# Optimization experiments

Measured on AMD Instinct MI355X. Metric: run time of the kernel, lower is better.

The kernel has to match this reference:

```python
import jax, jax.numpy as jnp
import numpy as np
from jax import lax

EPS = 1e-7  # keras.backend.epsilon()
DT = 0.05

def _k(a):
    # (3,3) -> HWIO (3,3,1,1) fp32 kernel constant
    return jnp.asarray(np.asarray(a, dtype=np.float32).reshape(3, 3, 1, 1))

KXP = _k([[0,0,0],[0,-1,1],[0,0,0]])
KXN = _k([[0,0,0],[-1,1,0],[0,0,0]])
KYP = _k([[0,1,0],[0,-1,0],[0,0,0]])
KYN = _k([[0,0,0],[0,1,0],[0,-1,0]])
KXC = _k([[0,0,0],[-1,0,1],[0,0,0]])
KYC = _k([[0,1,0],[0,0,0],[0,-1,0]])
KLX = _k([[1,0,-1],[2,0,-2],[1,0,-1]])
KLY = _k([[1,2,1],[0,0,0],[-1,-2,-1]])

def conv(x, k):
    # TF K.conv2d 'same' == XLA cross-correlation, NHWC/HWIO
    return lax.conv_general_dilated(x, k, (1, 1), 'SAME',
                                    dimension_numbers=('NHWC', 'HWIO', 'NHWC'))

def setup_inputs() -> dict:
    key = jax.random.key(0)
    k1, k2 = jax.random.split(key)
    B, H, W = 32, 512, 512
    u = jax.random.normal(k1, (B, H, W, 1), dtype=jnp.float32)
    img = jax.random.uniform(k2, (B, H, W, 1), dtype=jnp.float32)
    alpha = jnp.ones((1, 1, 1, 1), jnp.float32)
    beta = jnp.ones((1, 1, 1, 1), jnp.float32)
    gamma = jnp.ones((1, 1, 1, 1), jnp.float32)
    return {"u": u, "img": img, "alpha": alpha, "beta": beta, "gamma": gamma}

def reference(u, img, alpha, beta, gamma):
    # --- edge stopping function g(img) (precomputed in build() in original) ---
    ex = conv(img, KLX)
    ey = conv(img, KLY)
    edges = jnp.square(jnp.square(ex) + jnp.square(ey))
    edges = edges / jnp.max(edges)
    edges = 1.0 / (edges + 1.0)
    gex = conv(edges, KXC)
    gey = conv(edges, KYC)
    # --- upwind transport term ---
    xp = conv(u, KXP); xn = conv(u, KXN)
    yp = conv(u, KYP); yn = conv(u, KYN)
    fxp = jax.nn.relu(gex); fxn = -jax.nn.relu(-gex)
    fyp = jax.nn.relu(gey); fyn = -jax.nn.relu(-gey)
    transport = 20.0 * ((fxp * xp + fxn * xn) + (fyp * yp + fyn * yn))
    # --- curvature (divergence of normalized gradient) ---
    gux = conv(u, KXC)
    guy = conv(u, KYC)
    normu = jnp.sqrt(jnp.square(gux) + jnp.square(guy) + EPS)
    kappa = conv(gux / (normu + EPS), KXC) + conv(guy / (normu + EPS), KYC)
    curvature = edges * kappa * normu
    balloon = edges * normu
    return u + DT * (curvature * alpha + transport * beta + balloon * gamma)
```

## Files before the change

### kernel.cpp

```cpp
#include <hip/hip_runtime.h>

#define HH 512
#define WW 512
#define EPSF 1e-7f
#define DTF 0.05f
#define RS1 4
#define RSF 8
#define PANW 256

__device__ __forceinline__ float bperm(int addr, float v) {
    return __int_as_float(__builtin_amdgcn_ds_bpermute(addr, __float_as_int(v)));
}

struct R10 { float v[10]; };
struct Raw10 { float4 a, b; };

__device__ __forceinline__ void issue_row10(const float* __restrict__ base, int row,
                                            int lane, Raw10& r) {
    if ((unsigned)row < (unsigned)HH) {
        const float4* p = (const float4*)(base + (size_t)row * WW + 8 * lane);
        r.a = p[0]; r.b = p[1];
    } else {
        r.a = make_float4(0.f, 0.f, 0.f, 0.f);
        r.b = make_float4(0.f, 0.f, 0.f, 0.f);
    }
}

__device__ __forceinline__ void finish_row10(const Raw10& q, int bpu, int bpd,
                                             bool lo, bool hi, R10& r) {
    r.v[1] = q.a.x; r.v[2] = q.a.y; r.v[3] = q.a.z; r.v[4] = q.a.w;
    r.v[5] = q.b.x; r.v[6] = q.b.y; r.v[7] = q.b.z; r.v[8] = q.b.w;
    float l = bperm(bpu, r.v[8]);
    float h = bperm(bpd, r.v[1]);
    r.v[0] = lo ? 0.f : l;
    r.v[9] = hi ? 0.f : h;
}

__global__ __launch_bounds__(256, 4)
void max_e4_kernel(const float* __restrict__ img, float* __restrict__ partial) {
    const int wid  = blockIdx.x * 4 + (threadIdx.x >> 6);
    const int lane = threadIdx.x & 63;
    const int rs = wid & 127;
    const int b  = wid >> 7;
    const int i0 = rs * RS1;
    const float* __restrict__ IM = img + (size_t)b * (HH * WW);
    const bool lo = (lane == 0), hi = (lane == 63);
    const int bpu = ((lane + 63) & 63) << 2, bpd = ((lane + 1) & 63) << 2;

    Raw10 rA, rB;
    issue_row10(IM, i0 - 1, lane, rA);
    issue_row10(IM, i0,     lane, rB);
    R10 A, B, C;
    finish_row10(rA, bpu, bpd, lo, hi, A);
    issue_row10(IM, i0 + 1, lane, rA);
    finish_row10(rB, bpu, bpd, lo, hi, B);
    issue_row10(IM, i0 + 2, lane, rB);
    float m = 0.f;
    #pragma unroll
    for (int k = 0; k < RS1; ++k) {
        if (k & 1) {
            finish_row10(rB, bpu, bpd, lo, hi, C);
            if (k < RS1 - 2) issue_row10(IM, i0 + k + 3, lane, rB);
        } else {
            finish_row10(rA, bpu, bpd, lo, hi, C);
            if (k < RS1 - 2) issue_row10(IM, i0 + k + 3, lane, rA);
        }
        #pragma unroll
        for (int j = 1; j <= 8; ++j) {
            float ex = (A.v[j-1] - A.v[j+1]) + 2.f * (B.v[j-1] - B.v[j+1]) + (C.v[j-1] - C.v[j+1]);
            float ey = (A.v[j-1] - C.v[j-1]) + 2.f * (A.v[j] - C.v[j]) + (A.v[j+1] - C.v[j+1]);
            float s2 = ex * ex + ey * ey;
            m = fmaxf(m, s2 * s2);
        }
        A = B; B = C;
    }
    for (int off = 32; off > 0; off >>= 1)
        m = fmaxf(m, __shfl_down(m, off, 64));
    if (lane == 0) partial[wid] = m;
}

struct R7 { float v[6]; float x; };
struct RawR { float4 a; float2 t; };

__device__ __forceinline__ void issue_row(const float* __restrict__ base, int row,
                                          int lane, int c0, bool actL, bool actR, RawR& r) {
    if ((unsigned)row < (unsigned)HH) {
        const float* rp = base + (size_t)row * WW;
        r.a = *(const float4*)(rp + c0 + 4 * lane);
        if (actL | actR)
            r.t = *(const float2*)(rp + (actL ? c0 - 2 : c0 + PANW));
        else
            r.t = make_float2(0.f, 0.f);
    } else {
        r.a = make_float4(0.f, 0.f, 0.f, 0.f);
        r.t = make_float2(0.f, 0.f);
    }
}

__device__ __forceinline__ void finish_row(const RawR& q, int bpu, int bpd,
                                           bool actL, bool actR, bool zL, bool zR, R7& r) {
    r.v[1] = q.a.x; r.v[2] = q.a.y; r.v[3] = q.a.z; r.v[4] = q.a.w;
    float l = bperm(bpu, r.v[4]);
    float h = bperm(bpd, r.v[1]);
    float xx = 0.f;
    if (actL) { l = q.t.y; xx = q.t.x; }
    if (actR) { h = q.t.x; xx = q.t.y; }
    r.v[0] = zL ? 0.f : l;
    r.v[5] = zR ? 0.f : h;
    r.x = xx;
}

__global__ __launch_bounds__(256, 2)
void fused_ff(const float* __restrict__ u, const float* __restrict__ img,
              const float* __restrict__ pa, const float* __restrict__ pb,
              const float* __restrict__ pg, const float* __restrict__ partial,
              float* __restrict__ out) {
    __shared__ float sred[4];
    {
        float v = 0.f;
        #pragma unroll
        for (int k = 0; k < 16; ++k)
            v = fmaxf(v, partial[threadIdx.x + 256 * k]);
        for (int off = 32; off > 0; off >>= 1)
            v = fmaxf(v, __shfl_down(v, off, 64));
        if ((threadIdx.x & 63) == 0) sred[threadIdx.x >> 6] = v;
    }
    __syncthreads();
    const float M = fmaxf(fmaxf(sred[0], sred[1]), fmaxf(sred[2], sred[3]));

    const int wid  = blockIdx.x * 4 + (threadIdx.x >> 6);
    const int lane = threadIdx.x & 63;
    const int p  = wid & 1;
    const int rs = (wid >> 1) & 63;
    const int b  = wid >> 7;
    const int o0 = rs * RSF;
    const int c0 = p * PANW;
    const size_t base = (size_t)b * (HH * WW);
    const float* __restrict__ U  = u + base;
    const float* __restrict__ IM = img + base;
    float* __restrict__ O = out + base;
    const int bpu = ((lane + 63) & 63) << 2, bpd = ((lane + 1) & 63) << 2;
    const bool l0 = (lane == 0), l63 = (lane == 63);
    const bool actL = l0  && (c0 > 0);
    const bool actR = l63 && (c0 + PANW < WW);
    const bool zL = l0 && !actL, zR = l63 && !actR;

    const float dta = DTF * pa[0];
    const float dtb = 20.f * DTF * pb[0];
    const float dtg = DTF * pg[0];

    R7 I0 = {}, I1 = {}, R1 = {}, R2 = {};
    float E2[6] = {}, PX2[6] = {};
    float R0[5] = {}, E1[5] = {}, PY1[5] = {}, PY2[5] = {};

    if (o0 >= 2) {
        RawR q0i, q0u, q1i, q1u;
        issue_row(IM, o0 - 2, lane, c0, actL, actR, q0i);
        issue_row(U,  o0 - 2, lane, c0, actL, actR, q0u);
        issue_row(IM, o0 - 1, lane, c0, actL, actR, q1i);
        issue_row(U,  o0 - 1, lane, c0, actL, actR, q1u);
        finish_row(q0i, bpu, bpd, actL, actR, zL, zR, I0);
        finish_row(q0u, bpu, bpd, actL, actR, zL, zR, R1);
        finish_row(q1i, bpu, bpd, actL, actR, zL, zR, I1);
        finish_row(q1u, bpu, bpd, actL, actR, zL, zR, R2);
    }

    RawR pAi, pAu, pBi, pBu;
    issue_row(IM, o0,     lane, c0, actL, actR, pAi);
    issue_row(U,  o0,     lane, c0, actL, actR, pAu);
    issue_row(IM, o0 + 1, lane, c0, actL, actR, pBi);
    issue_row(U,  o0 + 1, lane, c0, actL, actR, pBu);

    #pragma unroll
    for (int kk = 0; kk < RSF + 2; ++kk) {
        const int o = o0 - 2 + kk;
        R7 C, W;
        if (kk & 1) {
            finish_row(pBi, bpu, bpd, actL, actR, zL, zR, C);
            finish_row(pBu, bpu, bpd, actL, actR, zL, zR, W);
            if (kk < RSF) {
                issue_row(IM, o0 + kk + 2, lane, c0, actL, actR, pBi);
                issue_row(U,  o0 + kk + 2, lane, c0, actL, actR, pBu);
            }
        } else {
            finish_row(pAi, bpu, bpd, actL, actR, zL, zR, C);
            finish_row(pAu, bpu, bpd, actL, actR, zL, zR, W);
            if (kk < RSF) {
                issue_row(IM, o0 + kk + 2, lane, c0, actL, actR, pAi);
                issue_row(U,  o0 + kk + 2, lane, c0, actL, actR, pAu);
            }
        }

        float eN[6], PXN[6], PYN[5];
        const bool rowv = (o >= -1) && (o < HH - 1);
        if (rowv) {
            #pragma unroll
            for (int k = 1; k <= 4; ++k) {
                float ex = (I0.v[k-1] - I0.v[k+1]) + 2.f * (I1.v[k-1] - I1.v[k+1]) + (C.v[k-1] - C.v[k+1]);
                float ey = (I0.v[k-1] - C.v[k-1]) + 2.f * (I0.v[k] - C.v[k]) + (I0.v[k+1] - C.v[k+1]);
                float s2 = ex * ex + ey * ey;
                eN[k] = M * __builtin_amdgcn_rcpf(s2 * s2 + M);
                float gux = R2.v[k+1] - R2.v[k-1];
                float guy = R1.v[k] - W.v[k];
                float rn  = __builtin_amdgcn_rsqf(gux * gux + guy * guy + EPSF);
                PXN[k] = gux * rn;
                PYN[k] = guy * rn;
            }
        } else {
            #pragma unroll
            for (int k = 1; k <= 4; ++k) { eN[k] = 0.f; PXN[k] = 0.f; PYN[k] = 0.f; }
        }
        {
            float a = bperm(bpu, eN[4]),  bb = bperm(bpd, eN[1]);
            float c = bperm(bpu, PXN[4]), d  = bperm(bpd, PXN[1]);
            eN[0]  = zL ? 0.f : a;  eN[5]  = zR ? 0.f : bb;
            PXN[0] = zL ? 0.f : c;  PXN[5] = zR ? 0.f : d;
        }
        if (rowv && (actL | actR)) {
            float i0a = actL ? I0.x    : I0.v[4];
            float i0b = actL ? I0.v[0] : I0.v[5];
            float i0c = actL ? I0.v[1] : I0.x;
            float i1a = actL ? I1.x    : I1.v[4];
            float i1c = actL ? I1.v[1] : I1.x;
            float ca  = actL ? C.x     : C.v[4];
            float cb  = actL ? C.v[0]  : C.v[5];
            float cc  = actL ? C.v[1]  : C.x;
            float ex = (i0a - i0c) + 2.f * (i1a - i1c) + (ca - cc);
            float ey = (i0a - ca) + 2.f * (i0b - cb) + (i0c - cc);
            float s2 = ex * ex + ey * ey;
            float eh = M * __builtin_amdgcn_rcpf(s2 * s2 + M);
            float gux = actL ? (R2.v[1] - R2.x)    : (R2.x - R2.v[4]);
            float guy = actL ? (R1.v[0] - W.v[0])  : (R1.v[5] - W.v[5]);
            float rn = __builtin_amdgcn_rsqf(gux * gux + guy * guy + EPSF);
            float ph = gux * rn;
            if (actL) { eN[0] = eh; PXN[0] = ph; }
            else      { eN[5] = eh; PXN[5] = ph; }
        }

        if (o >= o0) {
            float vals[4];
            #pragma unroll
            for (int k = 1; k <= 4; ++k) {
                float gex = E2[k+1] - E2[k-1];
                float gey = E1[k] - eN[k];
                float xp = R1.v[k+1] - R1.v[k], xn = R1.v[k] - R1.v[k-1];
                float yp = R0[k] - R1.v[k],     yn = R1.v[k] - R2.v[k];
                float tr = fmaxf(gex, 0.f) * xp + fminf(gex, 0.f) * xn
                         + fmaxf(gey, 0.f) * yp + fminf(gey, 0.f) * yn;
                float gxc = R1.v[k+1] - R1.v[k-1], gyc = R0[k] - R2.v[k];
                float ncv = __builtin_amdgcn_sqrtf(gxc * gxc + gyc * gyc + EPSF);
                float kap = (PX2[k+1] - PX2[k-1]) + (PY1[k] - PYN[k]);
                vals[k-1] = R1.v[k] + E2[k] * ncv * (kap * dta + dtg) + tr * dtb;
            }
            *(float4*)(O + (size_t)o * WW + c0 + 4 * lane) =
                make_float4(vals[0], vals[1], vals[2], vals[3]);
        }

        I0 = I1; I1 = C;
        #pragma unroll
        for (int k = 1; k <= 4; ++k) { R0[k] = R1.v[k]; E1[k] = E2[k]; PY1[k] = PY2[k]; PY2[k] = PYN[k]; }
        R1 = R2; R2 = W;
        #pragma unroll
        for (int k = 0; k < 6; ++k) { E2[k] = eN[k]; PX2[k] = PXN[k]; }
    }
}

extern "C" void kernel_launch(void* const* d_in, const int* in_sizes, int n_in,
                              void* d_out, int out_size, void* d_ws, size_t ws_size,
                              hipStream_t stream) {
    const float* u   = (const float*)d_in[0];
    const float* img = (const float*)d_in[1];
    const float* pa  = (const float*)d_in[2];
    const float* pb  = (const float*)d_in[3];
    const float* pg  = (const float*)d_in[4];
    float* out = (float*)d_out;
    float* partial = (float*)d_ws;

    max_e4_kernel<<<1024, 256, 0, stream>>>(img, partial);
    fused_ff<<<1024, 256, 0, stream>>>(u, img, pa, pb, pg, partial, out);
}
```

Measured before the change: 127.9 us.

## Replace cross-lane permutes with overlapping 8-wide halo loads and redundant halo compute

Each lane now loads its own two-column left and right halo (float2 + float4 + float2) from global memory instead of exchanging neighbor values with ds_bpermute. It also computes the edge and normalized-gradient terms for 6 columns instead of 4, so it no longer needs permutes for the derived halo or the special panel-boundary lane path. This removes LDS permute traffic and divergent boundary code. In exchange it issues extra, mostly cache-hit, global loads and adds about 50% more edge/rsq arithmetic per row.

```diff
diff --git a/kernel.cpp b/kernel.cpp
--- a/kernel.cpp
+++ b/kernel.cpp
@@ -79,35 +79,29 @@
     if (lane == 0) partial[wid] = m;
 }
 
-struct R7 { float v[6]; float x; };
-struct RawR { float4 a; float2 t; };
-
-__device__ __forceinline__ void issue_row(const float* __restrict__ base, int row,
-                                          int lane, int c0, bool actL, bool actR, RawR& r) {
+struct Raw8 { float2 L; float4 C4; float2 R; };
+struct W8 { float w[8]; };
+
+__device__ __forceinline__ void issue8(const float* __restrict__ base, int row,
+                                       int g, bool okL, bool okR, Raw8& r) {
     if ((unsigned)row < (unsigned)HH) {
         const float* rp = base + (size_t)row * WW;
-        r.a = *(const float4*)(rp + c0 + 4 * lane);
-        if (actL | actR)
-            r.t = *(const float2*)(rp + (actL ? c0 - 2 : c0 + PANW));
-        else
-            r.t = make_float2(0.f, 0.f);
+        r.L  = *(const float2*)(rp + (okL ? g - 2 : 0));
+        r.C4 = *(const float4*)(rp + g);
+        r.R  = *(const float2*)(rp + (okR ? g + 4 : WW - 2));
     } else {
-        r.a = make_float4(0.f, 0.f, 0.f, 0.f);
-        r.t = make_float2(0.f, 0.f);
-    }
-}
-
-__device__ __forceinline__ void finish_row(const RawR& q, int bpu, int bpd,
-                                           bool actL, bool actR, bool zL, bool zR, R7& r) {
-    r.v[1] = q.a.x; r.v[2] = q.a.y; r.v[3] = q.a.z; r.v[4] = q.a.w;
-    float l = bperm(bpu, r.v[4]);
-    float h = bperm(bpd, r.v[1]);
-    float xx = 0.f;
-    if (actL) { l = q.t.y; xx = q.t.x; }
-    if (actR) { h = q.t.x; xx = q.t.y; }
-    r.v[0] = zL ? 0.f : l;
-    r.v[5] = zR ? 0.f : h;
-    r.x = xx;
+        r.L  = make_float2(0.f, 0.f);
+        r.C4 = make_float4(0.f, 0.f, 0.f, 0.f);
+        r.R  = make_float2(0.f, 0.f);
+    }
+}
+
+__device__ __forceinline__ void finish8(const Raw8& q, bool okL, bool okR, W8& r) {
+    r.w[0] = okL ? q.L.x : 0.f;
+    r.w[1] = okL ? q.L.y : 0.f;
+    r.w[2] = q.C4.x; r.w[3] = q.C4.y; r.w[4] = q.C4.z; r.w[5] = q.C4.w;
+    r.w[6] = okR ? q.R.x : 0.f;
+    r.w[7] = okR ? q.R.y : 0.f;
 }
 
 __global__ __launch_bounds__(256, 2)
@@ -134,134 +128,115 @@
     const int rs = (wid >> 1) & 63;
     const int b  = wid >> 7;
     const int o0 = rs * RSF;
-    const int c0 = p * PANW;
+    const int g  = p * PANW + 4 * lane;
     const size_t base = (size_t)b * (HH * WW);
     const float* __restrict__ U  = u + base;
     const float* __restrict__ IM = img + base;
     float* __restrict__ O = out + base;
-    const int bpu = ((lane + 63) & 63) << 2, bpd = ((lane + 1) & 63) << 2;
-    const bool l0 = (lane == 0), l63 = (lane == 63);
-    const bool actL = l0  && (c0 > 0);
-    const bool actR = l63 && (c0 + PANW < WW);
-    const bool zL = l0 && !actL, zR = l63 && !actR;
+    const bool okL = (g >= 2);
+    const bool okR = (g + 5 < WW);
+    const bool ezL = (g == 0);
+    const bool ezR = (g + 4 >= WW);
 
     const float dta = DTF * pa[0];
     const float dtb = 20.f * DTF * pb[0];
     const float dtg = DTF * pg[0];
 
-    R7 I0 = {}, I1 = {}, R1 = {}, R2 = {};
-    float E2[6] = {}, PX2[6] = {};
-    float R0[5] = {}, E1[5] = {}, PY1[5] = {}, PY2[5] = {};
+    W8 I0 = {}, I1 = {}, R1 = {}, R2 = {};
+    float R0[4] = {}, E1c[4] = {}, E2[6] = {}, PX2[6] = {};
+    float PY1c[4] = {}, PY2c[4] = {};
 
     if (o0 >= 2) {
-        RawR q0i, q0u, q1i, q1u;
-        issue_row(IM, o0 - 2, lane, c0, actL, actR, q0i);
-        issue_row(U,  o0 - 2, lane, c0, actL, actR, q0u);
-        issue_row(IM, o0 - 1, lane, c0, actL, actR, q1i);
-        issue_row(U,  o0 - 1, lane, c0, actL, actR, q1u);
-        finish_row(q0i, bpu, bpd, actL, actR, zL, zR, I0);
-        finish_row(q0u, bpu, bpd, actL, actR, zL, zR, R1);
-        finish_row(q1i, bpu, bpd, actL, actR, zL, zR, I1);
-        finish_row(q1u, bpu, bpd, actL, actR, zL, zR, R2);
-    }
-
-    RawR pAi, pAu, pBi, pBu;
-    issue_row(IM, o0,     lane, c0, actL, actR, pAi);
-    issue_row(U,  o0,     lane, c0, actL, actR, pAu);
-    issue_row(IM, o0 + 1, lane, c0, actL, actR, pBi);
-    issue_row(U,  o0 + 1, lane, c0, actL, actR, pBu);
+        Raw8 qa, qb, qc, qd;
+        issue8(IM, o0 - 2, g, okL, okR, qa);
+        issue8(U,  o0 - 2, g, okL, okR, qb);
+        issue8(IM, o0 - 1, g, okL, okR, qc);
+        issue8(U,  o0 - 1, g, okL, okR, qd);
+        finish8(qa, okL, okR, I0);
+        finish8(qb, okL, okR, R1);
+        finish8(qc, okL, okR, I1);
+        finish8(qd, okL, okR, R2);
+    }
+
+    Raw8 pAi, pAu, pBi, pBu;
+    issue8(IM, o0,     g, okL, okR, pAi);
+    issue8(U,  o0,     g, okL, okR, pAu);
+    issue8(IM, o0 + 1, g, okL, okR, pBi);
+    issue8(U,  o0 + 1, g, okL, okR, pBu);
 
     #pragma unroll
     for (int kk = 0; kk < RSF + 2; ++kk) {
         const int o = o0 - 2 + kk;
-        R7 C, W;
+        W8 C, W;
         if (kk & 1) {
-            finish_row(pBi, bpu, bpd, actL, actR, zL, zR, C);
-            finish_row(pBu, bpu, bpd, actL, actR, zL, zR, W);
+            finish8(pBi, okL, okR, C);
+            finish8(pBu, okL, okR, W);
             if (kk < RSF) {
-                issue_row(IM, o0 + kk + 2, lane, c0, actL, actR, pBi);
-                issue_row(U,  o0 + kk + 2, lane, c0, actL, actR, pBu);
+                issue8(IM, o0 + kk + 2, g, okL, okR, pBi);
+                issue8(U,  o0 + kk + 2, g, okL, okR, pBu);
             }
         } else {
-            finish_row(pAi, bpu, bpd, actL, actR, zL, zR, C);
-            finish_row(pAu, bpu, bpd, actL, actR, zL, zR, W);
+            finish8(pAi, okL, okR, C);
+            finish8(pAu, okL, okR, W);
             if (kk < RSF) {
-                issue_row(IM, o0 + kk + 2, lane, c0, actL, actR, pAi);
-                issue_row(U,  o0 + kk + 2, lane, c0, actL, actR, pAu);
-            }
-        }
-
-        float eN[6], PXN[6], PYN[5];
+                issue8(IM, o0 + kk + 2, g, okL, okR, pAi);
+                issue8(U,  o0 + kk + 2, g, okL, okR, pAu);
+            }
+        }
+
+        float eN[6], PXN[6], PYNc[4];
         const bool rowv = (o >= -1) && (o < HH - 1);
         if (rowv) {
             #pragma unroll
-            for (int k = 1; k <= 4; ++k) {
-                float ex = (I0.v[k-1] - I0.v[k+1]) + 2.f * (I1.v[k-1] - I1.v[k+1]) + (C.v[k-1] - C.v[k+1]);
-                float ey = (I0.v[k-1] - C.v[k-1]) + 2.f * (I0.v[k] - C.v[k]) + (I0.v[k+1] - C.v[k+1]);
+            for (int i = 0; i < 6; ++i) {
+                float ex = (I0.w[i] - I0.w[i+2]) + 2.f * (I1.w[i] - I1.w[i+2]) + (C.w[i] - C.w[i+2]);
+                float ey = (I0.w[i] - C.w[i]) + 2.f * (I0.w[i+1] - C.w[i+1]) + (I0.w[i+2] - C.w[i+2]);
                 float s2 = ex * ex + ey * ey;
-                eN[k] = M * __builtin_amdgcn_rcpf(s2 * s2 + M);
-                float gux = R2.v[k+1] - R2.v[k-1];
-                float guy = R1.v[k] - W.v[k];
+                eN[i] = M * __builtin_amdgcn_rcpf(s2 * s2 + M);
+                float gux = R2.w[i+2] - R2.w[i];
+                float guy = R1.w[i+1] - W.w[i+1];
                 float rn  = __builtin_amdgcn_rsqf(gux * gux + guy * guy + EPSF);
-                PXN[k] = gux * rn;
-                PYN[k] = guy * rn;
-            }
+                PXN[i] = gux * rn;
+                if (i >= 1 && i <= 4) PYNc[i-1] = guy * rn;
+            }
+            if (ezL) { eN[0] = 0.f; PXN[0] = 0.f; }
+            if (ezR) { eN[5] = 0.f; PXN[5] = 0.f; }
         } else {
             #pragma unroll
-            for (int k = 1; k <= 4; ++k) { eN[k] = 0.f; PXN[k] = 0.f; PYN[k] = 0.f; }
-        }
-        {
-            float a = bperm(bpu, eN[4]),  bb = bperm(bpd, eN[1]);
-            float c = bperm(bpu, PXN[4]), d  = bperm(bpd, PXN[1]);
-            eN[0]  = zL ? 0.f : a;  eN[5]  = zR ? 0.f : bb;
-            PXN[0] = zL ? 0.f : c;  PXN[5] = zR ? 0.f : d;
-        }
-        if (rowv && (actL | actR)) {
-            float i0a = actL ? I0.x    : I0.v[4];
-            float i0b = actL ? I0.v[0] : I0.v[5];
-            float i0c = actL ? I0.v[1] : I0.x;
-            float i1a = actL ? I1.x    : I1.v[4];
-            float i1c = actL ? I1.v[1] : I1.x;
-            float ca  = actL ? C.x     : C.v[4];
-            float cb  = actL ? C.v[0]  : C.v[5];
-            float cc  = actL ? C.v[1]  : C.x;
-            float ex = (i0a - i0c) + 2.f * (i1a - i1c) + (ca - cc);
-            float ey = (i0a - ca) + 2.f * (i0b - cb) + (i0c - cc);
-            float s2 = ex * ex + ey * ey;
-            float eh = M * __builtin_amdgcn_rcpf(s2 * s2 + M);
-            float gux = actL ? (R2.v[1] - R2.x)    : (R2.x - R2.v[4]);
-            float guy = actL ? (R1.v[0] - W.v[0])  : (R1.v[5] - W.v[5]);
-            float rn = __builtin_amdgcn_rsqf(gux * gux + guy * guy + EPSF);
-            float ph = gux * rn;
-            if (actL) { eN[0] = eh; PXN[0] = ph; }
-            else      { eN[5] = eh; PXN[5] = ph; }
+            for (int i = 0; i < 6; ++i) { eN[i] = 0.f; PXN[i] = 0.f; }
+            #pragma unroll
+            for (int k = 0; k < 4; ++k) PYNc[k] = 0.f;
         }
 
         if (o >= o0) {
             float vals[4];
             #pragma unroll
-            for (int k = 1; k <= 4; ++k) {
-                float gex = E2[k+1] - E2[k-1];
-                float gey = E1[k] - eN[k];
-                float xp = R1.v[k+1] - R1.v[k], xn = R1.v[k] - R1.v[k-1];
-                float yp = R0[k] - R1.v[k],     yn = R1.v[k] - R2.v[k];
+            for (int k2 = 0; k2 < 4; ++k2) {
+                const int i = k2 + 1, j = k2 + 2;
+                float gex = E2[i+1] - E2[i-1];
+                float gey = E1c[k2] - eN[i];
+                float xp = R1.w[j+1] - R1.w[j], xn = R1.w[j] - R1.w[j-1];
+                float yp = R0[k2] - R1.w[j],    yn = R1.w[j] - R2.w[j];
                 float tr = fmaxf(gex, 0.f) * xp + fminf(gex, 0.f) * xn
                          + fmaxf(gey, 0.f) * yp + fminf(gey, 0.f) * yn;
-                float gxc = R1.v[k+1] - R1.v[k-1], gyc = R0[k] - R2.v[k];
+                float gxc = R1.w[j+1] - R1.w[j-1], gyc = R0[k2] - R2.w[j];
                 float ncv = __builtin_amdgcn_sqrtf(gxc * gxc + gyc * gyc + EPSF);
-                float kap = (PX2[k+1] - PX2[k-1]) + (PY1[k] - PYN[k]);
-                vals[k-1] = R1.v[k] + E2[k] * ncv * (kap * dta + dtg) + tr * dtb;
-            }
-            *(float4*)(O + (size_t)o * WW + c0 + 4 * lane) =
+                float kap = (PX2[i+1] - PX2[i-1]) + (PY1c[k2] - PYNc[k2]);
+                vals[k2] = R1.w[j] + E2[i] * ncv * (kap * dta + dtg) + tr * dtb;
+            }
+            *(float4*)(O + (size_t)o * WW + g) =
                 make_float4(vals[0], vals[1], vals[2], vals[3]);
         }
 
         I0 = I1; I1 = C;
         #pragma unroll
-        for (int k = 1; k <= 4; ++k) { R0[k] = R1.v[k]; E1[k] = E2[k]; PY1[k] = PY2[k]; PY2[k] = PYN[k]; }
+        for (int k2 = 0; k2 < 4; ++k2) {
+            R0[k2] = R1.w[k2+2]; E1c[k2] = E2[k2+1];
+            PY1c[k2] = PY2c[k2]; PY2c[k2] = PYNc[k2];
+        }
         R1 = R2; R2 = W;
         #pragma unroll
-        for (int k = 0; k < 6; ++k) { E2[k] = eN[k]; PX2[k] = PXN[k]; }
+        for (int i = 0; i < 6; ++i) { E2[i] = eN[i]; PX2[i] = PXN[i]; }
     }
 }
 
```

Result: faster. 124.7 us, median of 2 (-2.5%).
